# Kernel optimization log

Measured on AMD Instinct MI355X. Metric: run time of the kernel, lower is better.

Reference implementation:

```python
import jax, jax.numpy as jnp
import numpy as np

N = 50000      # total atoms/beads across batch
E = 800000     # total edges (avg degree 16)
H = 128        # hidden_channels
R = 50         # num_rbf
NB = 2         # n_interaction blocks
NG = 64        # num graphs in batch
NT = 100       # num atom types
CUT = 5.0      # upper distance cutoff


def setup_inputs() -> dict:
    key = jax.random.key(0)
    ks = jax.random.split(key, 20)
    atom_types = jax.random.randint(ks[0], (N,), 0, NT)
    pos = jax.random.uniform(ks[1], (N, 3), jnp.float32) * 30.0  # box of 30 Angstrom
    edge_index = jax.random.randint(ks[2], (2, E), 0, N)
    batch = jnp.sort(jax.random.randint(ks[3], (N,), 0, NG))

    def g(k, shape, fan_in):
        return jax.random.normal(k, shape, jnp.float32) * (1.0 / fan_in) ** 0.5

    emb = jax.random.normal(ks[4], (NT, H), jnp.float32) * 0.1
    # filter network per block: Linear(R->H) -> tanh -> Linear(H->H)
    fw1 = g(ks[5], (NB, R, H), R)
    fb1 = jnp.zeros((NB, H), jnp.float32)
    fw2 = g(ks[6], (NB, H, H), H)
    fb2 = jnp.zeros((NB, H), jnp.float32)
    # CFConv lin1 (no bias), lin2 (bias)
    lin1_w = g(ks[7], (NB, H, H), H)
    lin2_w = g(ks[8], (NB, H, H), H)
    lin2_b = jnp.zeros((NB, H), jnp.float32)
    # InteractionBlock output linear
    blk_w = g(ks[9], (NB, H, H), H)
    blk_b = jnp.zeros((NB, H), jnp.float32)
    # output network: Linear(H->H/2) -> tanh -> Linear(H/2->1)
    out_w1 = g(ks[10], (H, H // 2), H)
    out_b1 = jnp.zeros((H // 2,), jnp.float32)
    out_w2 = g(ks[11], (H // 2, 1), H // 2)
    out_b2 = jnp.zeros((1,), jnp.float32)
    return dict(atom_types=atom_types, pos=pos, edge_index=edge_index, batch=batch,
                emb=emb, fw1=fw1, fb1=fb1, fw2=fw2, fb2=fb2,
                lin1_w=lin1_w, lin2_w=lin2_w, lin2_b=lin2_b,
                blk_w=blk_w, blk_b=blk_b,
                out_w1=out_w1, out_b1=out_b1, out_w2=out_w2, out_b2=out_b2)


def reference(atom_types, pos, edge_index, batch, emb, fw1, fb1, fw2, fb2,
              lin1_w, lin2_w, lin2_b, blk_w, blk_b,
              out_w1, out_b1, out_w2, out_b2):
    src, dst = edge_index[0], edge_index[1]
    # pairwise distances along edges (eps keeps sqrt grad finite at coincident points)
    diff = pos[src] - pos[dst]                                  # [E,3]
    d = jnp.sqrt(jnp.sum(diff * diff, axis=-1) + 1e-12)         # [E]
    # Gaussian RBF expansion
    offsets = jnp.linspace(0.0, CUT, R)
    coeff = -0.5 / (offsets[1] - offsets[0]) ** 2
    rbf = jnp.exp(coeff * (d[:, None] - offsets) ** 2)          # [E,R]
    # cosine cutoff envelope
    Cenv = jnp.where(d < CUT, 0.5 * (jnp.cos(d * jnp.pi / CUT) + 1.0), 0.0)  # [E]

    x = emb[atom_types]                                          # [N,H]
    for i in range(NB):
        # filter generation from expanded distances
        W = jnp.tanh(rbf @ fw1[i] + fb1[i]) @ fw2[i] + fb2[i]    # [E,H]
        W = W * Cenv[:, None]
        # CFConv: lin1 -> gather*filter -> scatter-sum -> lin2
        h = x @ lin1_w[i]                                        # [N,H]
        msg = h[src] * W                                         # [E,H]
        agg = jax.ops.segment_sum(msg, dst, num_segments=N)      # [N,H]
        h = agg @ lin2_w[i] + lin2_b[i]
        # InteractionBlock: activation -> lin, residual add in SchNet.forward
        h = jnp.tanh(h)
        x = x + (h @ blk_w[i] + blk_b[i])
    # output network -> per-atom energy, scatter-sum per graph
    e = jnp.tanh(x @ out_w1 + out_b1) @ out_w2 + out_b2          # [N,1]
    energy = jax.ops.segment_sum(e, batch, num_segments=NG)      # [NG,1]
    return energy.flatten()
```

## Files before the change

### kernel.cpp

```cpp
#include <hip/hip_runtime.h>
#include <hip/hip_bf16.h>
#include <math.h>

#define H 128
#define RBF 50
#define CUTF 5.0f
#define PIF 3.14159265358979323846f
#define QT 1024
#define SEG 16

__global__ __launch_bounds__(256) void prep_kernel(
    const float* __restrict__ pos, float4* __restrict__ pos4, int Nn,
    int4* __restrict__ zbase, int zquads,
    const float* __restrict__ fw1, const float* __restrict__ fb1,
    const float* __restrict__ fw2, const float* __restrict__ fb2,
    const float* __restrict__ lin1w, const float* __restrict__ lin2b,
    const float* __restrict__ blkw, const float* __restrict__ blkb,
    const float* __restrict__ emb,
    const float* __restrict__ ow1, const float* __restrict__ ob1,
    const float* __restrict__ ow2, const float* __restrict__ ob2,
    float* __restrict__ tab, float* __restrict__ cvec,
    float* __restrict__ e_type, float* __restrict__ htype0,
    float* __restrict__ htype1, int NT,
    int ZFB, int PB, int FB, int TB, int H0B)
{
    int b = blockIdx.x;
    const int tid = threadIdx.x;
    const int lane = tid & 63;

    if (b < ZFB) {
        int i = b * 256 + tid;
        if (i < zquads) zbase[i] = make_int4(0, 0, 0, 0);
        return;
    }
    b -= ZFB;
    if (b < PB) {
        int n = b * 256 + tid;
        if (n < Nn)
            pos4[n] = make_float4(pos[3 * n], pos[3 * n + 1], pos[3 * n + 2], 0.0f);
        return;
    }
    b -= PB;
    const int h0 = lane, h1 = lane + 64;
    if (b < FB) {
        const int wid = b * 4 + (tid >> 6);
        const int ntab = 2 * (QT + 1);
        if (wid >= ntab + 2) return;
        if (wid >= ntab) {
            const int blk = wid - ntab;
            const float* bwp = blkw + (size_t)blk * H * H;
            float t0 = tanhf(lin2b[blk * H + h0]);
            float t1 = tanhf(lin2b[blk * H + h1]);
            float a0 = blkb[blk * H + h0], a1 = blkb[blk * H + h1];
            #pragma unroll 8
            for (int k = 0; k < 64; ++k) {
                float bb2 = __shfl(t0, k, 64);
                a0 = fmaf(bb2, bwp[k * H + h0], a0);
                a1 = fmaf(bb2, bwp[k * H + h1], a1);
            }
            #pragma unroll 8
            for (int k = 0; k < 64; ++k) {
                float bb2 = __shfl(t1, k, 64);
                a0 = fmaf(bb2, bwp[(64 + k) * H + h0], a0);
                a1 = fmaf(bb2, bwp[(64 + k) * H + h1], a1);
            }
            cvec[blk * H + h0] = a0;
            cvec[blk * H + h1] = a1;
            return;
        }
        const int blk = wid / (QT + 1);
        const int q = wid - blk * (QT + 1);
        const float d = (float)q * (CUTF / (float)QT);
        const float* f1 = fw1 + (size_t)blk * RBF * H;
        const float* f2 = fw2 + (size_t)blk * H * H;
        const float step  = CUTF / 49.0f;
        const float coeff = -0.5f / (step * step);
        float cenv = (d < CUTF) ? 0.5f * (cosf(d * (PIF / CUTF)) + 1.0f) : 0.0f;

        float t0 = fb1[blk * H + h0], t1 = fb1[blk * H + h1];
        #pragma unroll
        for (int r = 0; r < RBF; ++r) {
            float u = d - (float)r * step;
            float rb = expf(coeff * u * u);
            t0 = fmaf(rb, f1[r * H + h0], t0);
            t1 = fmaf(rb, f1[r * H + h1], t1);
        }
        t0 = tanhf(t0); t1 = tanhf(t1);
        float w0 = fb2[blk * H + h0], w1v = fb2[blk * H + h1];
        #pragma unroll 8
        for (int k = 0; k < 64; ++k) {
            float bb2 = __shfl(t0, k, 64);
            w0  = fmaf(bb2, f2[k * H + h0], w0);
            w1v = fmaf(bb2, f2[k * H + h1], w1v);
        }
        #pragma unroll 8
        for (int k = 0; k < 64; ++k) {
            float bb2 = __shfl(t1, k, 64);
            w0  = fmaf(bb2, f2[(64 + k) * H + h0], w0);
            w1v = fmaf(bb2, f2[(64 + k) * H + h1], w1v);
        }
        float* row = tab + ((size_t)blk * (QT + 1) + q) * H;
        row[h0] = w0 * cenv;
        row[h1] = w1v * cenv;
        return;
    }
    b -= FB;
    if (b < TB) {
        const int ty = b * 4 + (tid >> 6);
        if (ty >= NT) return;
        float xt0 = emb[(size_t)ty * H + h0];
        float xt1 = emb[(size_t)ty * H + h1];
        #pragma unroll
        for (int blk = 0; blk < 2; ++blk) {
            const float* bwp = blkw + (size_t)blk * H * H;
            float t0 = tanhf(lin2b[blk * H + h0]);
            float t1 = tanhf(lin2b[blk * H + h1]);
            float a0 = blkb[blk * H + h0], a1 = blkb[blk * H + h1];
            #pragma unroll 8
            for (int k = 0; k < 64; ++k) {
                float bb2 = __shfl(t0, k, 64);
                a0 = fmaf(bb2, bwp[k * H + h0], a0);
                a1 = fmaf(bb2, bwp[k * H + h1], a1);
            }
            #pragma unroll 8
            for (int k = 0; k < 64; ++k) {
                float bb2 = __shfl(t1, k, 64);
                a0 = fmaf(bb2, bwp[(64 + k) * H + h0], a0);
                a1 = fmaf(bb2, bwp[(64 + k) * H + h1], a1);
            }
            xt0 += a0; xt1 += a1;
        }
        float y = ob1[lane];
        #pragma unroll 8
        for (int k = 0; k < 64; ++k) {
            float bb2 = __shfl(xt0, k, 64);
            y = fmaf(bb2, ow1[k * 64 + lane], y);
        }
        #pragma unroll 8
        for (int k = 0; k < 64; ++k) {
            float bb2 = __shfl(xt1, k, 64);
            y = fmaf(bb2, ow1[(64 + k) * 64 + lane], y);
        }
        y = tanhf(y) * ow2[lane];
        #pragma unroll
        for (int off = 32; off; off >>= 1) y += __shfl_xor(y, off, 64);
        if (lane == 0) e_type[ty] = y + ob2[0];
        return;
    }
    b -= TB;
    if (b < H0B) {
        const int ty = b * 4 + (tid >> 6);
        if (ty >= NT) return;
        float x0 = emb[(size_t)ty * H + h0];
        float x1 = emb[(size_t)ty * H + h1];
        float a0 = 0.f, a1 = 0.f;
        #pragma unroll 8
        for (int k = 0; k < 64; ++k) {
            float bb2 = __shfl(x0, k, 64);
            a0 = fmaf(bb2, lin1w[k * H + h0], a0);
            a1 = fmaf(bb2, lin1w[k * H + h1], a1);
        }
        #pragma unroll 8
        for (int k = 0; k < 64; ++k) {
            float bb2 = __shfl(x1, k, 64);
            a0 = fmaf(bb2, lin1w[(64 + k) * H + h0], a0);
            a1 = fmaf(bb2, lin1w[(64 + k) * H + h1], a1);
        }
        htype0[(size_t)ty * H + h0] = a0;
        htype0[(size_t)ty * H + h1] = a1;
        return;
    }
    b -= H0B;
    {
        const int ty = b * 4 + (tid >> 6);
        if (ty >= NT) return;
        const float* bwp = blkw;
        float t0 = tanhf(lin2b[h0]);
        float t1 = tanhf(lin2b[h1]);
        float c0 = blkb[h0], c1 = blkb[h1];
        #pragma unroll 8
        for (int k = 0; k < 64; ++k) {
            float bb2 = __shfl(t0, k, 64);
            c0 = fmaf(bb2, bwp[k * H + h0], c0);
            c1 = fmaf(bb2, bwp[k * H + h1], c1);
        }
        #pragma unroll 8
        for (int k = 0; k < 64; ++k) {
            float bb2 = __shfl(t1, k, 64);
            c0 = fmaf(bb2, bwp[(64 + k) * H + h0], c0);
            c1 = fmaf(bb2, bwp[(64 + k) * H + h1], c1);
        }
        float x0 = emb[(size_t)ty * H + h0] + c0;
        float x1 = emb[(size_t)ty * H + h1] + c1;
        const float* l1 = lin1w + (size_t)H * H;
        float a0 = 0.f, a1 = 0.f;
        #pragma unroll 8
        for (int k = 0; k < 64; ++k) {
            float bb2 = __shfl(x0, k, 64);
            a0 = fmaf(bb2, l1[k * H + h0], a0);
            a1 = fmaf(bb2, l1[k * H + h1], a1);
        }
        #pragma unroll 8
        for (int k = 0; k < 64; ++k) {
            float bb2 = __shfl(x1, k, 64);
            a0 = fmaf(bb2, l1[(64 + k) * H + h0], a0);
            a1 = fmaf(bb2, l1[(64 + k) * H + h1], a1);
        }
        htype1[(size_t)ty * H + h0] = a0;
        htype1[(size_t)ty * H + h1] = a1;
    }
}

__global__ __launch_bounds__(256) void edge_prep_kernel(
    const float4* __restrict__ pos4, const int* __restrict__ ei,
    const int* __restrict__ atype, int E, int CAP,
    int* __restrict__ seg_cnt, int* __restrict__ asrc, int* __restrict__ adst,
    float* __restrict__ ad, int* __restrict__ asty,
    int* __restrict__ is_src, int* __restrict__ is_dst)
{
    __shared__ int wtot[4], wbase[4];
    const int tid = threadIdx.x;
    const int lane = tid & 63;
    const int wv = tid >> 6;
    const int gtid = blockIdx.x * 256 + tid;

    int s[4], t[4];
    float d[4];
    bool act[4] = {false, false, false, false};

    const int e0 = gtid * 4;
    if (e0 + 3 < E && (E & 3) == 0) {
        const int4 sv = *(const int4*)(ei + e0);
        const int4 tv = *(const int4*)(ei + E + e0);
        s[0] = sv.x; s[1] = sv.y; s[2] = sv.z; s[3] = sv.w;
        t[0] = tv.x; t[1] = tv.y; t[2] = tv.z; t[3] = tv.w;
        #pragma unroll
        for (int j = 0; j < 4; ++j) {
            float4 ps = pos4[s[j]], pt = pos4[t[j]];
            float dx = ps.x - pt.x, dy = ps.y - pt.y, dz = ps.z - pt.z;
            d[j] = sqrtf(dx * dx + dy * dy + dz * dz + 1e-12f);
            act[j] = (d[j] < CUTF);
        }
    } else if (e0 < E) {
        #pragma unroll
        for (int j = 0; j < 4; ++j) {
            int e = e0 + j;
            if (e < E) {
                s[j] = ei[e]; t[j] = ei[E + e];
                float4 ps = pos4[s[j]], pt = pos4[t[j]];
                float dx = ps.x - pt.x, dy = ps.y - pt.y, dz = ps.z - pt.z;
                d[j] = sqrtf(dx * dx + dy * dy + dz * dz + 1e-12f);
                act[j] = (d[j] < CUTF);
            }
        }
    }

    unsigned long long b[4];
    int mytot = 0;
    #pragma unroll
    for (int j = 0; j < 4; ++j) {
        b[j] = __ballot(act[j]);
        mytot += (int)__popcll(b[j]);
    }
    if (lane == 0) wtot[wv] = mytot;
    __syncthreads();
    if (tid == 0) {
        int t0 = wtot[0], t1 = wtot[1], t2 = wtot[2], t3 = wtot[3];
        int tot = t0 + t1 + t2 + t3;
        int base = 0;
        if (tot) base = atomicAdd(&seg_cnt[blockIdx.x & (SEG - 1)], tot);
        wbase[0] = base; wbase[1] = base + t0;
        wbase[2] = base + t0 + t1; wbase[3] = base + t0 + t1 + t2;
    }
    __syncthreads();

    int run = wbase[wv];
    const int segoff = (int)(blockIdx.x & (SEG - 1)) * CAP;
    const unsigned long long ltm = ((unsigned long long)1 << lane) - 1;
    #pragma unroll
    for (int j = 0; j < 4; ++j) {
        if (act[j]) {
            int p = segoff + run + (int)__popcll(b[j] & ltm);
            asrc[p] = s[j]; adst[p] = t[j]; ad[p] = d[j];
            asty[p] = atype[s[j]];
            is_src[s[j]] = 1; is_dst[t[j]] = 1;
        }
        run += (int)__popcll(b[j]);
    }
}

__global__ __launch_bounds__(256) void compact_atoms_kernel(
    const int* __restrict__ is_src, const int* __restrict__ is_dst, int Nn,
    int* __restrict__ cnt4,
    int* __restrict__ dst_list, int* __restrict__ sd_list,
    float* __restrict__ agg)
{
    __shared__ int wtot[2][4], wbase[2][4];
    const int tid = threadIdx.x;
    const int lane = tid & 63;
    const int wv = tid >> 6;
    int n = blockIdx.x * 256 + tid;
    bool v[2] = {false, false};
    if (n < Nn) {
        bool vd = is_dst[n] != 0;
        v[0] = vd;
        v[1] = vd && (is_src[n] != 0);
    }
    unsigned long long b[2];
    #pragma unroll
    for (int l = 0; l < 2; ++l) {
        b[l] = __ballot(v[l]);
        if (lane == 0) wtot[l][wv] = (int)__popcll(b[l]);
    }
    __syncthreads();
    if (tid == 0) {
        #pragma unroll
        for (int l = 0; l < 2; ++l) {
            int t0 = wtot[l][0], t1 = wtot[l][1], t2 = wtot[l][2], t3 = wtot[l][3];
            int tot = t0 + t1 + t2 + t3;
            int base = 0;
            if (tot) base = atomicAdd(cnt4 + 1 + l, tot);
            wbase[l][0] = base; wbase[l][1] = base + t0;
            wbase[l][2] = base + t0 + t1; wbase[l][3] = base + t0 + t1 + t2;
        }
    }
    __syncthreads();
    const unsigned long long ltm = ((unsigned long long)1 << lane) - 1;
    if (v[0]) dst_list[wbase[0][wv] + (int)__popcll(b[0] & ltm)] = n;
    if (v[1]) sd_list[wbase[1][wv] + (int)__popcll(b[1] & ltm)] = n;
    if (v[0]) {
        float4 z = make_float4(0.f, 0.f, 0.f, 0.f);
        float4* row = (float4*)(agg + (size_t)n * H);
        #pragma unroll
        for (int c = 0; c < 32; ++c) row[c] = z;
    }
}

__global__ __launch_bounds__(256) void edge_scatter0_kernel(
    const int* __restrict__ seg_cnt,
    const int* __restrict__ adst, const float* __restrict__ ad,
    const int* __restrict__ asty, const float* __restrict__ tab,
    const float* __restrict__ htype0, float* __restrict__ agg, int CAP)
{
    __shared__ int sbase[SEG + 1];
    const int tid = threadIdx.x;
    if (tid == 0) {
        int run = 0;
        #pragma unroll
        for (int s2 = 0; s2 < SEG; ++s2) { sbase[s2] = run; run += seg_cnt[s2]; }
        sbase[SEG] = run;
    }
    __syncthreads();

    const int lane = tid & 63;
    const int wid = (blockIdx.x * blockDim.x + tid) >> 6;
    const int nw  = (gridDim.x * blockDim.x) >> 6;
    const int total = sbase[SEG];
    const float scale = (float)QT / CUTF;

    for (int i = wid; i < total; i += nw) {
        int seg = 0;
        #pragma unroll
        for (int s2 = 1; s2 < SEG; ++s2) seg += (i >= sbase[s2]) ? 1 : 0;
        int slot = seg * CAP + (i - sbase[seg]);

        int t = adst[slot];
        int ty = asty[slot];
        float p = ad[slot] * scale;
        int i0 = (int)p;
        if (i0 > QT - 1) i0 = QT - 1;
        float f = p - (float)i0;
        const float* r0 = tab + (size_t)i0 * H;
        float wl = fmaf(f, r0[H + lane] - r0[lane], r0[lane]);
        float wh = fmaf(f, r0[H + 64 + lane] - r0[64 + lane], r0[64 + lane]);
        const float* hr = htype0 + (size_t)ty * H;
        atomicAdd(agg + (size_t)t * H + lane, hr[lane] * wl);
        atomicAdd(agg + (size_t)t * H + 64 + lane, hr[64 + lane] * wh);
    }
}

__global__ __launch_bounds__(256) void edge_scatter1_kernel(
    const int* __restrict__ seg_cnt,
    const int* __restrict__ asrc, const int* __restrict__ adst,
    const float* __restrict__ ad, const int* __restrict__ asty,
    const int* __restrict__ is_dst, const float* __restrict__ tab,
    const float* __restrict__ hbuf, const float* __restrict__ htype1,
    float* __restrict__ agg, int CAP)
{
    __shared__ int sbase[SEG + 1];
    const int tid = threadIdx.x;
    if (tid == 0) {
        int run = 0;
        #pragma unroll
        for (int s2 = 0; s2 < SEG; ++s2) { sbase[s2] = run; run += seg_cnt[s2]; }
        sbase[SEG] = run;
    }
    __syncthreads();

    const int lane = tid & 63;
    const int wid = (blockIdx.x * blockDim.x + tid) >> 6;
    const int nw  = (gridDim.x * blockDim.x) >> 6;
    const int total = sbase[SEG];
    const float scale = (float)QT / CUTF;

    for (int i = wid; i < total; i += nw) {
        int seg = 0;
        #pragma unroll
        for (int s2 = 1; s2 < SEG; ++s2) seg += (i >= sbase[s2]) ? 1 : 0;
        int slot = seg * CAP + (i - sbase[seg]);

        int s = asrc[slot];
        int t = adst[slot];
        float p = ad[slot] * scale;
        int i0 = (int)p;
        if (i0 > QT - 1) i0 = QT - 1;
        float f = p - (float)i0;
        const float* r0 = tab + (size_t)i0 * H;
        float wl = fmaf(f, r0[H + lane] - r0[lane], r0[lane]);
        float wh = fmaf(f, r0[H + 64 + lane] - r0[64 + lane], r0[64 + lane]);
        const float* hr = is_dst[s] ? (hbuf + (size_t)s * H)
                                    : (htype1 + (size_t)asty[slot] * H);
        atomicAdd(agg + (size_t)t * H + lane, hr[lane] * wl);
        atomicAdd(agg + (size_t)t * H + 64 + lane, hr[64 + lane] * wh);
    }
}

__global__ __launch_bounds__(256) void gemm_sd_kernel(
    const float* __restrict__ A, const float* __restrict__ W,
    float* __restrict__ C,
    const int* __restrict__ rows, const int* __restrict__ cntp)
{
    __shared__ float As[32][36];
    __shared__ float Ws[32][128];
    __shared__ int rlist[32];

    const int tid = threadIdx.x;
    const int cnt = *cntp;
    const int r0 = (tid >> 4) * 2;
    const int c0 = (tid & 15) * 4;

    for (int tile = blockIdx.x; tile * 32 < cnt; tile += gridDim.x) {
        __syncthreads();
        if (tid < 32) {
            int idx = tile * 32 + tid;
            rlist[tid] = (idx < cnt) ? rows[idx] : -1;
        }
        __syncthreads();

        float acc[2][8];
        #pragma unroll
        for (int j = 0; j < 2; ++j)
            #pragma unroll
            for (int c = 0; c < 8; ++c) acc[j][c] = 0.f;

        for (int kc = 0; kc < H; kc += 32) {
            {
                int lr = tid >> 3;
                int kk = (tid & 7) * 4;
                int r = rlist[lr];
                float4 v = make_float4(0.f, 0.f, 0.f, 0.f);
                if (r >= 0) v = *(const float4*)(A + (size_t)r * H + kc + kk);
                *(float4*)&As[lr][kk] = v;
            }
            {
                int wr = tid >> 5;
                int wc = (tid & 31) * 4;
                #pragma unroll
                for (int p = 0; p < 4; ++p) {
                    int row = wr + p * 8;
                    *(float4*)&Ws[row][wc] = *(const float4*)(W + (size_t)(kc + row) * H + wc);
                }
            }
            __syncthreads();
            #pragma unroll
            for (int k = 0; k < 32; k += 4) {
                float a_[2][4];
                #pragma unroll
                for (int j = 0; j < 2; ++j)
                    *(float4*)a_[j] = *(const float4*)&As[r0 + j][k];
                #pragma unroll
                for (int kk = 0; kk < 4; ++kk) {
                    float4 wlo = *(const float4*)&Ws[k + kk][c0];
                    float4 whi = *(const float4*)&Ws[k + kk][c0 + 64];
                    float w_[8] = {wlo.x, wlo.y, wlo.z, wlo.w, whi.x, whi.y, whi.z, whi.w};
                    #pragma unroll
                    for (int j = 0; j < 2; ++j)
                        #pragma unroll
                        for (int c = 0; c < 8; ++c)
                            acc[j][c] = fmaf(a_[j][kk], w_[c], acc[j][c]);
                }
            }
            __syncthreads();
        }
        #pragma unroll
        for (int j = 0; j < 2; ++j) {
            int r = rlist[r0 + j];
            if (r < 0) continue;
            #pragma unroll
            for (int hh = 0; hh < 2; ++hh) {
                int cb = c0 + hh * 64;
                *(float4*)(C + (size_t)r * H + cb) = make_float4(
                    acc[j][hh * 4 + 0], acc[j][hh * 4 + 1],
                    acc[j][hh * 4 + 2], acc[j][hh * 4 + 3]);
            }
        }
    }
}

__global__ __launch_bounds__(256) void update_x0_kernel(
    float* __restrict__ agg, const float* __restrict__ l2w,
    const float* __restrict__ l2b, const float* __restrict__ bw,
    const float* __restrict__ bb, float* __restrict__ x,
    const float* __restrict__ emb, const int* __restrict__ atype,
    const int* __restrict__ rows, const int* __restrict__ cntp)
{
    __shared__ float As[32][36];
    __shared__ float Ws[32][128];
    __shared__ float Tl[32][132];
    __shared__ int rlist[32], tlist[32];

    const int tid = threadIdx.x;
    const int cnt = *cntp;
    const int r0 = (tid >> 4) * 2;
    const int c0 = (tid & 15) * 4;

    for (int tile = blockIdx.x; tile * 32 < cnt; tile += gridDim.x) {
        __syncthreads();
        if (tid < 32) {
            int idx = tile * 32 + tid;
            int r = (idx < cnt) ? rows[idx] : -1;
            rlist[tid] = r;
            tlist[tid] = (r >= 0) ? atype[r] : 0;
        }
        __syncthreads();

        float acc[2][8];
        #pragma unroll
        for (int j = 0; j < 2; ++j)
            #pragma unroll
            for (int c = 0; c < 8; ++c) acc[j][c] = 0.f;

        for (int kc = 0; kc < H; kc += 32) {
            {
                int lr = tid >> 3;
                int kk = (tid & 7) * 4;
                int r = rlist[lr];
                float4 v = make_float4(0.f, 0.f, 0.f, 0.f);
                if (r >= 0) v = *(const float4*)(agg + (size_t)r * H + kc + kk);
                *(float4*)&As[lr][kk] = v;
            }
            {
                int wr = tid >> 5;
                int wc = (tid & 31) * 4;
                #pragma unroll
                for (int p = 0; p < 4; ++p) {
                    int row = wr + p * 8;
                    *(float4*)&Ws[row][wc] = *(const float4*)(l2w + (size_t)(kc + row) * H + wc);
                }
            }
            __syncthreads();
            #pragma unroll
            for (int k = 0; k < 32; k += 4) {
                float a_[2][4];
                #pragma unroll
                for (int j = 0; j < 2; ++j)
                    *(float4*)a_[j] = *(const float4*)&As[r0 + j][k];
                #pragma unroll
                for (int kk = 0; kk < 4; ++kk) {
                    float4 wlo = *(const float4*)&Ws[k + kk][c0];
                    float4 whi = *(const float4*)&Ws[k + kk][c0 + 64];
                    float w_[8] = {wlo.x, wlo.y, wlo.z, wlo.w, whi.x, whi.y, whi.z, whi.w};
                    #pragma unroll
                    for (int j = 0; j < 2; ++j)
                        #pragma unroll
                        for (int c = 0; c < 8; ++c)
                            acc[j][c] = fmaf(a_[j][kk], w_[c], acc[j][c]);
                }
            }
            __syncthreads();
        }
        {
            float4 z = make_float4(0.f, 0.f, 0.f, 0.f);
            for (int idx = tid; idx < 32 * 32; idx += 256) {
                int row = idx >> 5, c = (idx & 31) << 2;
                int r = rlist[row];
                if (r >= 0) *(float4*)(agg + (size_t)r * H + c) = z;
            }
        }
        #pragma unroll
        for (int j = 0; j < 2; ++j) {
            float4 lo, hi;
            lo.x = tanhf(acc[j][0] + l2b[c0]);      lo.y = tanhf(acc[j][1] + l2b[c0 + 1]);
            lo.z = tanhf(acc[j][2] + l2b[c0 + 2]);  lo.w = tanhf(acc[j][3] + l2b[c0 + 3]);
            hi.x = tanhf(acc[j][4] + l2b[c0 + 64]); hi.y = tanhf(acc[j][5] + l2b[c0 + 65]);
            hi.z = tanhf(acc[j][6] + l2b[c0 + 66]); hi.w = tanhf(acc[j][7] + l2b[c0 + 67]);
            *(float4*)&Tl[r0 + j][c0] = lo;
            *(float4*)&Tl[r0 + j][c0 + 64] = hi;
        }

        float acc2[2][8];
        #pragma unroll
        for (int j = 0; j < 2; ++j)
            #pragma unroll
            for (int c = 0; c < 8; ++c) acc2[j][c] = 0.f;

        for (int kc = 0; kc < H; kc += 32) {
            __syncthreads();
            {
                int wr = tid >> 5;
                int wc = (tid & 31) * 4;
                #pragma unroll
                for (int p = 0; p < 4; ++p) {
                    int row = wr + p * 8;
                    *(float4*)&Ws[row][wc] = *(const float4*)(bw + (size_t)(kc + row) * H + wc);
                }
            }
            __syncthreads();
            #pragma unroll
            for (int k = 0; k < 32; k += 4) {
                float a_[2][4];
                #pragma unroll
                for (int j = 0; j < 2; ++j)
                    *(float4*)a_[j] = *(const float4*)&Tl[r0 + j][kc + k];
                #pragma unroll
                for (int kk = 0; kk < 4; ++kk) {
                    float4 wlo = *(const float4*)&Ws[k + kk][c0];
                    float4 whi = *(const float4*)&Ws[k + kk][c0 + 64];
                    float w_[8] = {wlo.x, wlo.y, wlo.z, wlo.w, whi.x, whi.y, whi.z, whi.w};
                    #pragma unroll
                    for (int j = 0; j < 2; ++j)
                        #pragma unroll
                        for (int c = 0; c < 8; ++c)
                            acc2[j][c] = fmaf(a_[j][kk], w_[c], acc2[j][c]);
                }
            }
        }
        #pragma unroll
        for (int j = 0; j < 2; ++j) {
            int r = rlist[r0 + j];
            if (r < 0) continue;
            int ty = tlist[r0 + j];
            #pragma unroll
            for (int hh = 0; hh < 2; ++hh) {
                int cb = c0 + hh * 64;
                float4 xv = *(const float4*)(emb + (size_t)ty * H + cb);
                xv.x += acc2[j][hh * 4 + 0] + bb[cb];
                xv.y += acc2[j][hh * 4 + 1] + bb[cb + 1];
                xv.z += acc2[j][hh * 4 + 2] + bb[cb + 2];
                xv.w += acc2[j][hh * 4 + 3] + bb[cb + 3];
                *(float4*)(x + (size_t)r * H + cb) = xv;
            }
        }
    }
}

__global__ __launch_bounds__(256) void update_e_kernel(
    const float* __restrict__ agg, const float* __restrict__ l2w,
    const float* __restrict__ l2b, const float* __restrict__ bw,
    const float* __restrict__ bb, const float* __restrict__ x,
    const float* __restrict__ ow1, const float* __restrict__ ob1,
    const float* __restrict__ ow2, const float* __restrict__ ob2,
    float* __restrict__ e_atom,
    const int* __restrict__ rows, const int* __restrict__ cntp)
{
    __shared__ float As[32][36];
    __shared__ float Ws[32][128];
    __shared__ float Tl[32][132];
    __shared__ int rlist[32];

    const int tid = threadIdx.x;
    const int cnt = *cntp;
    const int r0 = (tid >> 4) * 2;
    const int c0 = (tid & 15) * 4;

    for (int tile = blockIdx.x; tile * 32 < cnt; tile += gridDim.x) {
        __syncthreads();
        if (tid < 32) {
            int idx = tile * 32 + tid;
            rlist[tid] = (idx < cnt) ? rows[idx] : -1;
        }
        __syncthreads();

        float acc[2][8];
        #pragma unroll
        for (int j = 0; j < 2; ++j)
            #pragma unroll
            for (int c = 0; c < 8; ++c) acc[j][c] = 0.f;

        for (int kc = 0; kc < H; kc += 32) {
            {
                int lr = tid >> 3;
                int kk = (tid & 7) * 4;
                int r = rlist[lr];
                float4 v = make_float4(0.f, 0.f, 0.f, 0.f);
                if (r >= 0) v = *(const float4*)(agg + (size_t)r * H + kc + kk);
                *(float4*)&As[lr][kk] = v;
            }
            {
                int wr = tid >> 5;
                int wc = (tid & 31) * 4;
                #pragma unroll
                for (int p = 0; p < 4; ++p) {
                    int row = wr + p * 8;
                    *(float4*)&Ws[row][wc] = *(const float4*)(l2w + (size_t)(kc + row) * H + wc);
                }
            }
            __syncthreads();
            #pragma unroll
            for (int k = 0; k < 32; k += 4) {
                float a_[2][4];
                #pragma unroll
                for (int j = 0; j < 2; ++j)
                    *(float4*)a_[j] = *(const float4*)&As[r0 + j][k];
                #pragma unroll
                for (int kk = 0; kk < 4; ++kk) {
                    float4 wlo = *(const float4*)&Ws[k + kk][c0];
                    float4 whi = *(const float4*)&Ws[k + kk][c0 + 64];
                    float w_[8] = {wlo.x, wlo.y, wlo.z, wlo.w, whi.x, whi.y, whi.z, whi.w};
                    #pragma unroll
                    for (int j = 0; j < 2; ++j)
                        #pragma unroll
                        for (int c = 0; c < 8; ++c)
                            acc[j][c] = fmaf(a_[j][kk], w_[c], acc[j][c]);
                }
            }
            __syncthreads();
        }
        #pragma unroll
        for (int j = 0; j < 2; ++j) {
            float4 lo, hi;
            lo.x = tanhf(acc[j][0] + l2b[c0]);      lo.y = tanhf(acc[j][1] + l2b[c0 + 1]);
            lo.z = tanhf(acc[j][2] + l2b[c0 + 2]);  lo.w = tanhf(acc[j][3] + l2b[c0 + 3]);
            hi.x = tanhf(acc[j][4] + l2b[c0 + 64]); hi.y = tanhf(acc[j][5] + l2b[c0 + 65]);
            hi.z = tanhf(acc[j][6] + l2b[c0 + 66]); hi.w = tanhf(acc[j][7] + l2b[c0 + 67]);
            *(float4*)&Tl[r0 + j][c0] = lo;
            *(float4*)&Tl[r0 + j][c0 + 64] = hi;
        }

        float acc2[2][8];
        #pragma unroll
        for (int j = 0; j < 2; ++j)
            #pragma unroll
            for (int c = 0; c < 8; ++c) acc2[j][c] = 0.f;

        for (int kc = 0; kc < H; kc += 32) {
            __syncthreads();
            {
                int wr = tid >> 5;
                int wc = (tid & 31) * 4;
                #pragma unroll
                for (int p = 0; p < 4; ++p) {
                    int row = wr + p * 8;
                    *(float4*)&Ws[row][wc] = *(const float4*)(bw + (size_t)(kc + row) * H + wc);
                }
            }
            __syncthreads();
            #pragma unroll
            for (int k = 0; k < 32; k += 4) {
                float a_[2][4];
                #pragma unroll
                for (int j = 0; j < 2; ++j)
                    *(float4*)a_[j] = *(const float4*)&Tl[r0 + j][kc + k];
                #pragma unroll
                for (int kk = 0; kk < 4; ++kk) {
                    float4 wlo = *(const float4*)&Ws[k + kk][c0];
                    float4 whi = *(const float4*)&Ws[k + kk][c0 + 64];
                    float w_[8] = {wlo.x, wlo.y, wlo.z, wlo.w, whi.x, whi.y, whi.z, whi.w};
                    #pragma unroll
                    for (int j = 0; j < 2; ++j)
                        #pragma unroll
                        for (int c = 0; c < 8; ++c)
                            acc2[j][c] = fmaf(a_[j][kk], w_[c], acc2[j][c]);
                }
            }
        }
        __syncthreads();
        #pragma unroll
        for (int j = 0; j < 2; ++j) {
            int r = rlist[r0 + j];
            #pragma unroll
            for (int hh = 0; hh < 2; ++hh) {
                int cb = c0 + hh * 64;
                float4 xv = make_float4(0.f, 0.f, 0.f, 0.f);
                if (r >= 0) xv = *(const float4*)(x + (size_t)r * H + cb);
                xv.x += acc2[j][hh * 4 + 0] + bb[cb];
                xv.y += acc2[j][hh * 4 + 1] + bb[cb + 1];
                xv.z += acc2[j][hh * 4 + 2] + bb[cb + 2];
                xv.w += acc2[j][hh * 4 + 3] + bb[cb + 3];
                *(float4*)&Tl[r0 + j][cb] = xv;
            }
        }

        float acc3[2][4];
        #pragma unroll
        for (int j = 0; j < 2; ++j)
            #pragma unroll
            for (int c = 0; c < 4; ++c) acc3[j][c] = 0.f;

        for (int kc = 0; kc < H; kc += 32) {
            __syncthreads();
            {
                int wr = tid >> 4;
                int wc = (tid & 15) * 4;
                #pragma unroll
                for (int p = 0; p < 2; ++p) {
                    int row = wr + p * 16;
                    *(float4*)&Ws[row][wc] = *(const float4*)(ow1 + (size_t)(kc + row) * 64 + wc);
                }
            }
            __syncthreads();
            #pragma unroll
            for (int k = 0; k < 32; ++k) {
                float a_[2];
                #pragma unroll
                for (int j = 0; j < 2; ++j) a_[j] = Tl[r0 + j][kc + k];
                float4 wv = *(const float4*)&Ws[k][c0];
                #pragma unroll
                for (int j = 0; j < 2; ++j) {
                    acc3[j][0] = fmaf(a_[j], wv.x, acc3[j][0]);
                    acc3[j][1] = fmaf(a_[j], wv.y, acc3[j][1]);
                    acc3[j][2] = fmaf(a_[j], wv.z, acc3[j][2]);
                    acc3[j][3] = fmaf(a_[j], wv.w, acc3[j][3]);
                }
            }
        }
        const float4 b1v = *(const float4*)(ob1 + c0);
        const float4 w2v = *(const float4*)(ow2 + c0);
        float ep[2];
        #pragma unroll
        for (int j = 0; j < 2; ++j) {
            float v0 = tanhf(acc3[j][0] + b1v.x);
            float v1 = tanhf(acc3[j][1] + b1v.y);
            float v2 = tanhf(acc3[j][2] + b1v.z);
            float v3 = tanhf(acc3[j][3] + b1v.w);
            ep[j] = v0 * w2v.x + v1 * w2v.y + v2 * w2v.z + v3 * w2v.w;
        }
        #pragma unroll
        for (int off = 1; off < 16; off <<= 1) {
            ep[0] += __shfl_xor(ep[0], off, 64);
            ep[1] += __shfl_xor(ep[1], off, 64);
        }
        if ((tid & 15) == 0) {
            const float b2v = ob2[0];
            #pragma unroll
            for (int j = 0; j < 2; ++j) {
                int r = rlist[r0 + j];
                if (r >= 0) e_atom[r] = ep[j] + b2v;
            }
        }
    }
}

__global__ __launch_bounds__(256) void energy_graph_kernel(
    const int* __restrict__ batch, const int* __restrict__ atype,
    const int* __restrict__ is_dst, const float* __restrict__ e_atom,
    const float* __restrict__ e_type, float* __restrict__ energy, int Nn)
{
    const int g = blockIdx.x;
    int lo = 0, hi = Nn;
    while (lo < hi) { int m = (lo + hi) >> 1; if (batch[m] < g) lo = m + 1; else hi = m; }
    const int start = lo;
    hi = Nn;
    while (lo < hi) { int m = (lo + hi) >> 1; if (batch[m] < g + 1) lo = m + 1; else hi = m; }
    const int end = lo;

    float s = 0.0f;
    for (int n = start + (int)threadIdx.x; n < end; n += 256)
        s += is_dst[n] ? e_atom[n] : e_type[atype[n]];
    #pragma unroll
    for (int off = 32; off; off >>= 1) s += __shfl_xor(s, off, 64);
    __shared__ float wp[4];
    if ((threadIdx.x & 63) == 0) wp[threadIdx.x >> 6] = s;
    __syncthreads();
    if (threadIdx.x == 0) energy[g] = wp[0] + wp[1] + wp[2] + wp[3];
}

extern "C" void kernel_launch(void* const* d_in, const int* in_sizes, int n_in,
                              void* d_out, int out_size, void* d_ws, size_t ws_size,
                              hipStream_t stream)
{
    const int*   atype = (const int*)  d_in[0];
    const float* pos   = (const float*)d_in[1];
    const int*   ei    = (const int*)  d_in[2];
    const int*   batch = (const int*)  d_in[3];
    const float* emb   = (const float*)d_in[4];
    const float* fw1   = (const float*)d_in[5];
    const float* fb1   = (const float*)d_in[6];
    const float* fw2   = (const float*)d_in[7];
    const float* fb2   = (const float*)d_in[8];
    const float* lin1w = (const float*)d_in[9];
    const float* lin2w = (const float*)d_in[10];
    const float* lin2b = (const float*)d_in[11];
    const float* blkw  = (const float*)d_in[12];
    const float* blkb  = (const float*)d_in[13];
    const float* ow1   = (const float*)d_in[14];
    const float* ob1   = (const float*)d_in[15];
    const float* ow2   = (const float*)d_in[16];
    const float* ob2   = (const float*)d_in[17];

    const int Nn = in_sizes[0];
    const int E  = in_sizes[2] / 2;
    const int NT = in_sizes[4] / H;
    float* energy = (float*)d_out;

    const int eblocks = (E + 1023) / 1024;
    const int bps = (eblocks + SEG - 1) / SEG;
    const int CAP = bps * 1024;
    const int SEGCAP = SEG * CAP;

    char* w = (char*)d_ws;
    int*   cnt  = (int*)w;
    int*   seg_cnt = cnt + 8;
    int*   is_src = cnt + 32;
    int*   is_dst = is_src + Nn;
    float* x    = (float*)(is_dst + Nn);
    float* hbuf = x + (size_t)Nn * H;
    float* agg  = hbuf + (size_t)Nn * H;
    int*   asrc = (int*)(agg + (size_t)Nn * H);
    int*   adst = asrc + SEGCAP;
    float* ad   = (float*)(adst + SEGCAP);
    int*   asty = (int*)(ad + SEGCAP);
    int*   dst_list = asty + SEGCAP;
    int*   sd_list  = dst_list + Nn;
    float* cvec = (float*)(sd_list + Nn);
    float* tab  = cvec + 2 * H;
    float* e_type = tab + 2 * (size_t)(QT + 1) * H;
    float* htype0 = e_type + 128;
    float* htype1 = htype0 + (size_t)NT * H;
    float* e_atom = htype1 + (size_t)NT * H;
    float4* pos4 = (float4*)(e_atom + Nn);

    const int zquads = (128 + 2 * Nn * 4) / 16;
    const int ZFB = (zquads + 255) / 256;
    const int PB  = (Nn + 255) / 256;
    const int FB  = (2 * (QT + 1) + 2 + 3) / 4;
    const int TB  = (NT + 3) / 4;
    const int H0B = (NT + 3) / 4;
    const int H1B = (NT + 3) / 4;

    prep_kernel<<<ZFB + PB + FB + TB + H0B + H1B, 256, 0, stream>>>(
        pos, pos4, Nn, (int4*)cnt, zquads,
        fw1, fb1, fw2, fb2, lin1w, lin2b, blkw, blkb, emb,
        ow1, ob1, ow2, ob2, tab, cvec, e_type, htype0, htype1, NT,
        ZFB, PB, FB, TB, H0B);

    edge_prep_kernel<<<eblocks, 256, 0, stream>>>(
        pos4, ei, atype, E, CAP, seg_cnt, asrc, adst, ad, asty, is_src, is_dst);
    compact_atoms_kernel<<<(Nn + 255) / 256, 256, 0, stream>>>(
        is_src, is_dst, Nn, cnt, dst_list, sd_list, agg);

    edge_scatter0_kernel<<<1024, 256, 0, stream>>>(
        seg_cnt, adst, ad, asty, tab, htype0, agg, CAP);
    update_x0_kernel<<<512, 256, 0, stream>>>(
        agg, lin2w, lin2b, blkw, blkb, x, emb, atype, dst_list, cnt + 1);

    gemm_sd_kernel<<<128, 256, 0, stream>>>(
        x, lin1w + (size_t)H * H, hbuf, sd_list, cnt + 2);
    edge_scatter1_kernel<<<1024, 256, 0, stream>>>(
        seg_cnt, asrc, adst, ad, asty, is_dst,
        tab + (size_t)(QT + 1) * H, hbuf, htype1, agg, CAP);
    update_e_kernel<<<512, 256, 0, stream>>>(
        agg, lin2w + (size_t)H * H, lin2b + H, blkw + (size_t)H * H, blkb + H,
        x, ow1, ob1, ow2, ob2, e_atom, dst_list, cnt + 1);

    energy_graph_kernel<<<out_size, 256, 0, stream>>>(
        batch, atype, is_dst, e_atom, e_type, energy, Nn);
}
```

Before: 223.2 us.

## Fuse atom compaction into scatter0 and lin1 GEMM into update_x0

Merges compact_atoms into the first edge-scatter launch as extra blocks, and moves zeroing of agg into the prep kernel's bulk zero-fill. Fuses the block-1 lin1 GEMM (x @ lin1_w) into update_x0, so the freshly updated x tile is reused from shared memory instead of being re-read by a separate gemm_sd kernel. Removes the unused cvec precompute. This cuts two kernel launches and one N×H read of x, at the cost of zero-filling all of agg (not just dst rows) and extra work for atoms that are not sources.

```diff
diff --git a/kernel.cpp b/kernel.cpp
--- a/kernel.cpp
+++ b/kernel.cpp
@@ -8,6 +8,7 @@
 #define PIF 3.14159265358979323846f
 #define QT 1024
 #define SEG 16
+#define SB 1024
 
 __global__ __launch_bounds__(256) void prep_kernel(
     const float* __restrict__ pos, float4* __restrict__ pos4, int Nn,
@@ -19,9 +20,8 @@
     const float* __restrict__ emb,
     const float* __restrict__ ow1, const float* __restrict__ ob1,
     const float* __restrict__ ow2, const float* __restrict__ ob2,
-    float* __restrict__ tab, float* __restrict__ cvec,
-    float* __restrict__ e_type, float* __restrict__ htype0,
-    float* __restrict__ htype1, int NT,
+    float* __restrict__ tab, float* __restrict__ e_type,
+    float* __restrict__ htype0, float* __restrict__ htype1, int NT,
     int ZFB, int PB, int FB, int TB, int H0B)
 {
     int b = blockIdx.x;
@@ -45,29 +45,7 @@
     if (b < FB) {
         const int wid = b * 4 + (tid >> 6);
         const int ntab = 2 * (QT + 1);
-        if (wid >= ntab + 2) return;
-        if (wid >= ntab) {
-            const int blk = wid - ntab;
-            const float* bwp = blkw + (size_t)blk * H * H;
-            float t0 = tanhf(lin2b[blk * H + h0]);
-            float t1 = tanhf(lin2b[blk * H + h1]);
-            float a0 = blkb[blk * H + h0], a1 = blkb[blk * H + h1];
-            #pragma unroll 8
-            for (int k = 0; k < 64; ++k) {
-                float bb2 = __shfl(t0, k, 64);
-                a0 = fmaf(bb2, bwp[k * H + h0], a0);
-                a1 = fmaf(bb2, bwp[k * H + h1], a1);
-            }
-            #pragma unroll 8
-            for (int k = 0; k < 64; ++k) {
-                float bb2 = __shfl(t1, k, 64);
-                a0 = fmaf(bb2, bwp[(64 + k) * H + h0], a0);
-                a1 = fmaf(bb2, bwp[(64 + k) * H + h1], a1);
-            }
-            cvec[blk * H + h0] = a0;
-            cvec[blk * H + h1] = a1;
-            return;
-        }
+        if (wid >= ntab) return;
         const int blk = wid / (QT + 1);
         const int q = wid - blk * (QT + 1);
         const float d = (float)q * (CUTF / (float)QT);
@@ -289,61 +267,53 @@
     }
 }
 
-__global__ __launch_bounds__(256) void compact_atoms_kernel(
-    const int* __restrict__ is_src, const int* __restrict__ is_dst, int Nn,
-    int* __restrict__ cnt4,
-    int* __restrict__ dst_list, int* __restrict__ sd_list,
-    float* __restrict__ agg)
-{
-    __shared__ int wtot[2][4], wbase[2][4];
-    const int tid = threadIdx.x;
-    const int lane = tid & 63;
-    const int wv = tid >> 6;
-    int n = blockIdx.x * 256 + tid;
-    bool v[2] = {false, false};
-    if (n < Nn) {
-        bool vd = is_dst[n] != 0;
-        v[0] = vd;
-        v[1] = vd && (is_src[n] != 0);
-    }
-    unsigned long long b[2];
-    #pragma unroll
-    for (int l = 0; l < 2; ++l) {
-        b[l] = __ballot(v[l]);
-        if (lane == 0) wtot[l][wv] = (int)__popcll(b[l]);
-    }
-    __syncthreads();
-    if (tid == 0) {
-        #pragma unroll
-        for (int l = 0; l < 2; ++l) {
-            int t0 = wtot[l][0], t1 = wtot[l][1], t2 = wtot[l][2], t3 = wtot[l][3];
-            int tot = t0 + t1 + t2 + t3;
-            int base = 0;
-            if (tot) base = atomicAdd(cnt4 + 1 + l, tot);
-            wbase[l][0] = base; wbase[l][1] = base + t0;
-            wbase[l][2] = base + t0 + t1; wbase[l][3] = base + t0 + t1 + t2;
-        }
-    }
-    __syncthreads();
-    const unsigned long long ltm = ((unsigned long long)1 << lane) - 1;
-    if (v[0]) dst_list[wbase[0][wv] + (int)__popcll(b[0] & ltm)] = n;
-    if (v[1]) sd_list[wbase[1][wv] + (int)__popcll(b[1] & ltm)] = n;
-    if (v[0]) {
-        float4 z = make_float4(0.f, 0.f, 0.f, 0.f);
-        float4* row = (float4*)(agg + (size_t)n * H);
-        #pragma unroll
-        for (int c = 0; c < 32; ++c) row[c] = z;
-    }
-}
-
-__global__ __launch_bounds__(256) void edge_scatter0_kernel(
+__global__ __launch_bounds__(256) void scatter0_compact_kernel(
     const int* __restrict__ seg_cnt,
     const int* __restrict__ adst, const float* __restrict__ ad,
     const int* __restrict__ asty, const float* __restrict__ tab,
-    const float* __restrict__ htype0, float* __restrict__ agg, int CAP)
+    const float* __restrict__ htype0, float* __restrict__ agg, int CAP,
+    const int* __restrict__ is_src, const int* __restrict__ is_dst, int Nn,
+    int* __restrict__ cnt4, int* __restrict__ dst_list, int* __restrict__ sd_list)
 {
+    const int tid = threadIdx.x;
+    const int lane = tid & 63;
+
+    if (blockIdx.x >= SB) {
+        __shared__ int wtot[2][4], wbase[2][4];
+        const int wv = tid >> 6;
+        int n = ((int)blockIdx.x - SB) * 256 + tid;
+        bool v[2] = {false, false};
+        if (n < Nn) {
+            bool vd = is_dst[n] != 0;
+            v[0] = vd;
+            v[1] = vd && (is_src[n] != 0);
+        }
+        unsigned long long b[2];
+        #pragma unroll
+        for (int l = 0; l < 2; ++l) {
+            b[l] = __ballot(v[l]);
+            if (lane == 0) wtot[l][wv] = (int)__popcll(b[l]);
+        }
+        __syncthreads();
+        if (tid == 0) {
+            #pragma unroll
+            for (int l = 0; l < 2; ++l) {
+                int t0 = wtot[l][0], t1 = wtot[l][1], t2 = wtot[l][2], t3 = wtot[l][3];
+                int tot = t0 + t1 + t2 + t3;
+                int base = 0;
+                if (tot) base = atomicAdd(cnt4 + 1 + l, tot);
+                wbase[l][0] = base; wbase[l][1] = base + t0;
+                wbase[l][2] = base + t0 + t1; wbase[l][3] = base + t0 + t1 + t2;
+            }
+        }
+        __syncthreads();
+        const unsigned long long ltm = ((unsigned long long)1 << lane) - 1;
+        if (v[0]) dst_list[wbase[0][wv] + (int)__popcll(b[0] & ltm)] = n;
+        if (v[1]) sd_list[wbase[1][wv] + (int)__popcll(b[1] & ltm)] = n;
+        return;
+    }
+
     __shared__ int sbase[SEG + 1];
-    const int tid = threadIdx.x;
     if (tid == 0) {
         int run = 0;
         #pragma unroll
@@ -352,9 +322,8 @@
     }
     __syncthreads();
 
-    const int lane = tid & 63;
     const int wid = (blockIdx.x * blockDim.x + tid) >> 6;
-    const int nw  = (gridDim.x * blockDim.x) >> 6;
+    const int nw  = (SB * 256) >> 6;
     const int total = sbase[SEG];
     const float scale = (float)QT / CUTF;
 
@@ -425,14 +394,19 @@
     }
 }
 
-__global__ __launch_bounds__(256) void gemm_sd_kernel(
-    const float* __restrict__ A, const float* __restrict__ W,
-    float* __restrict__ C,
+__global__ __launch_bounds__(256) void update_x0_kernel(
+    float* __restrict__ agg, const float* __restrict__ l2w,
+    const float* __restrict__ l2b, const float* __restrict__ bw,
+    const float* __restrict__ bb, float* __restrict__ x,
+    const float* __restrict__ emb, const int* __restrict__ atype,
+    const int* __restrict__ is_src, const float* __restrict__ l1w1,
+    float* __restrict__ hbuf,
     const int* __restrict__ rows, const int* __restrict__ cntp)
 {
     __shared__ float As[32][36];
     __shared__ float Ws[32][128];
-    __shared__ int rlist[32];
+    __shared__ float Tl[32][132];
+    __shared__ int rlist[32], tlist[32], slist[32];
 
     const int tid = threadIdx.x;
     const int cnt = *cntp;
@@ -443,7 +417,10 @@
         __syncthreads();
         if (tid < 32) {
             int idx = tile * 32 + tid;
-            rlist[tid] = (idx < cnt) ? rows[idx] : -1;
+            int r = (idx < cnt) ? rows[idx] : -1;
+            rlist[tid] = r;
+            tlist[tid] = (r >= 0) ? atype[r] : 0;
+            slist[tid] = (r >= 0) ? is_src[r] : 0;
         }
         __syncthreads();
 
@@ -459,7 +436,7 @@
                 int kk = (tid & 7) * 4;
                 int r = rlist[lr];
                 float4 v = make_float4(0.f, 0.f, 0.f, 0.f);
-                if (r >= 0) v = *(const float4*)(A + (size_t)r * H + kc + kk);
+                if (r >= 0) v = *(const float4*)(agg + (size_t)r * H + kc + kk);
                 *(float4*)&As[lr][kk] = v;
             }
             {
@@ -468,7 +445,7 @@
                 #pragma unroll
                 for (int p = 0; p < 4; ++p) {
                     int row = wr + p * 8;
-                    *(float4*)&Ws[row][wc] = *(const float4*)(W + (size_t)(kc + row) * H + wc);
+                    *(float4*)&Ws[row][wc] = *(const float4*)(l2w + (size_t)(kc + row) * H + wc);
                 }
             }
             __syncthreads();
@@ -492,93 +469,6 @@
             }
             __syncthreads();
         }
-        #pragma unroll
-        for (int j = 0; j < 2; ++j) {
-            int r = rlist[r0 + j];
-            if (r < 0) continue;
-            #pragma unroll
-            for (int hh = 0; hh < 2; ++hh) {
-                int cb = c0 + hh * 64;
-                *(float4*)(C + (size_t)r * H + cb) = make_float4(
-                    acc[j][hh * 4 + 0], acc[j][hh * 4 + 1],
-                    acc[j][hh * 4 + 2], acc[j][hh * 4 + 3]);
-            }
-        }
-    }
-}
-
-__global__ __launch_bounds__(256) void update_x0_kernel(
-    float* __restrict__ agg, const float* __restrict__ l2w,
-    const float* __restrict__ l2b, const float* __restrict__ bw,
-    const float* __restrict__ bb, float* __restrict__ x,
-    const float* __restrict__ emb, const int* __restrict__ atype,
-    const int* __restrict__ rows, const int* __restrict__ cntp)
-{
-    __shared__ float As[32][36];
-    __shared__ float Ws[32][128];
-    __shared__ float Tl[32][132];
-    __shared__ int rlist[32], tlist[32];
-
-    const int tid = threadIdx.x;
-    const int cnt = *cntp;
-    const int r0 = (tid >> 4) * 2;
-    const int c0 = (tid & 15) * 4;
-
-    for (int tile = blockIdx.x; tile * 32 < cnt; tile += gridDim.x) {
-        __syncthreads();
-        if (tid < 32) {
-            int idx = tile * 32 + tid;
-            int r = (idx < cnt) ? rows[idx] : -1;
-            rlist[tid] = r;
-            tlist[tid] = (r >= 0) ? atype[r] : 0;
-        }
-        __syncthreads();
-
-        float acc[2][8];
-        #pragma unroll
-        for (int j = 0; j < 2; ++j)
-            #pragma unroll
-            for (int c = 0; c < 8; ++c) acc[j][c] = 0.f;
-
-        for (int kc = 0; kc < H; kc += 32) {
-            {
-                int lr = tid >> 3;
-                int kk = (tid & 7) * 4;
-                int r = rlist[lr];
-                float4 v = make_float4(0.f, 0.f, 0.f, 0.f);
-                if (r >= 0) v = *(const float4*)(agg + (size_t)r * H + kc + kk);
-                *(float4*)&As[lr][kk] = v;
-            }
-            {
-                int wr = tid >> 5;
-                int wc = (tid & 31) * 4;
-                #pragma unroll
-                for (int p = 0; p < 4; ++p) {
-                    int row = wr + p * 8;
-                    *(float4*)&Ws[row][wc] = *(const float4*)(l2w + (size_t)(kc + row) * H + wc);
-                }
-            }
-            __syncthreads();
-            #pragma unroll
-            for (int k = 0; k < 32; k += 4) {
-                float a_[2][4];
-                #pragma unroll
-                for (int j = 0; j < 2; ++j)
-                    *(float4*)a_[j] = *(const float4*)&As[r0 + j][k];
-                #pragma unroll
-                for (int kk = 0; kk < 4; ++kk) {
-                    float4 wlo = *(const float4*)&Ws[k + kk][c0];
-                    float4 whi = *(const float4*)&Ws[k + kk][c0 + 64];
-                    float w_[8] = {wlo.x, wlo.y, wlo.z, wlo.w, whi.x, whi.y, whi.z, whi.w};
-                    #pragma unroll
-                    for (int j = 0; j < 2; ++j)
-                        #pragma unroll
-                        for (int c = 0; c < 8; ++c)
-                            acc[j][c] = fmaf(a_[j][kk], w_[c], acc[j][c]);
-                }
-            }
-            __syncthreads();
-        }
         {
             float4 z = make_float4(0.f, 0.f, 0.f, 0.f);
             for (int idx = tid; idx < 32 * 32; idx += 256) {
@@ -635,20 +525,72 @@
                 }
             }
         }
+        __syncthreads();
         #pragma unroll
         for (int j = 0; j < 2; ++j) {
             int r = rlist[r0 + j];
-            if (r < 0) continue;
             int ty = tlist[r0 + j];
             #pragma unroll
             for (int hh = 0; hh < 2; ++hh) {
                 int cb = c0 + hh * 64;
-                float4 xv = *(const float4*)(emb + (size_t)ty * H + cb);
+                float4 xv = make_float4(0.f, 0.f, 0.f, 0.f);
+                if (r >= 0) xv = *(const float4*)(emb + (size_t)ty * H + cb);
                 xv.x += acc2[j][hh * 4 + 0] + bb[cb];
                 xv.y += acc2[j][hh * 4 + 1] + bb[cb + 1];
                 xv.z += acc2[j][hh * 4 + 2] + bb[cb + 2];
                 xv.w += acc2[j][hh * 4 + 3] + bb[cb + 3];
-                *(float4*)(x + (size_t)r * H + cb) = xv;
+                *(float4*)&Tl[r0 + j][cb] = xv;
+                if (r >= 0) *(float4*)(x + (size_t)r * H + cb) = xv;
+            }
+        }
+
+        float acc3[2][8];
+        #pragma unroll
+        for (int j = 0; j < 2; ++j)
+            #pragma unroll
+            for (int c = 0; c < 8; ++c) acc3[j][c] = 0.f;
+
+        for (int kc = 0; kc < H; kc += 32) {
+            __syncthreads();
+            {
+                int wr = tid >> 5;
+                int wc = (tid & 31) * 4;
+                #pragma unroll
+                for (int p = 0; p < 4; ++p) {
+                    int row = wr + p * 8;
+                    *(float4*)&Ws[row][wc] = *(const float4*)(l1w1 + (size_t)(kc + row) * H + wc);
+                }
+            }
+            __syncthreads();
+            #pragma unroll
+            for (int k = 0; k < 32; k += 4) {
+                float a_[2][4];
+                #pragma unroll
+                for (int j = 0; j < 2; ++j)
+                    *(float4*)a_[j] = *(const float4*)&Tl[r0 + j][kc + k];
+                #pragma unroll
+                for (int kk = 0; kk < 4; ++kk) {
+                    float4 wlo = *(const float4*)&Ws[k + kk][c0];
+                    float4 whi = *(const float4*)&Ws[k + kk][c0 + 64];
+                    float w_[8] = {wlo.x, wlo.y, wlo.z, wlo.w, whi.x, whi.y, whi.z, whi.w};
+                    #pragma unroll
+                    for (int j = 0; j < 2; ++j)
+                        #pragma unroll
+                        for (int c = 0; c < 8; ++c)
+                            acc3[j][c] = fmaf(a_[j][kk], w_[c], acc3[j][c]);
+                }
+            }
+        }
+        #pragma unroll
+        for (int j = 0; j < 2; ++j) {
+            int r = rlist[r0 + j];
+            if (r < 0 || !slist[r0 + j]) continue;
+            #pragma unroll
+            for (int hh = 0; hh < 2; ++hh) {
+                int cb = c0 + hh * 64;
+                *(float4*)(hbuf + (size_t)r * H + cb) = make_float4(
+                    acc3[j][hh * 4 + 0], acc3[j][hh * 4 + 1],
+                    acc3[j][hh * 4 + 2], acc3[j][hh * 4 + 3]);
             }
         }
     }
@@ -913,27 +855,27 @@
     int*   seg_cnt = cnt + 8;
     int*   is_src = cnt + 32;
     int*   is_dst = is_src + Nn;
-    float* x    = (float*)(is_dst + Nn);
+    float* agg  = (float*)(is_dst + Nn);
+    float* x    = agg + (size_t)Nn * H;
     float* hbuf = x + (size_t)Nn * H;
-    float* agg  = hbuf + (size_t)Nn * H;
-    int*   asrc = (int*)(agg + (size_t)Nn * H);
+    int*   asrc = (int*)(hbuf + (size_t)Nn * H);
     int*   adst = asrc + SEGCAP;
     float* ad   = (float*)(adst + SEGCAP);
     int*   asty = (int*)(ad + SEGCAP);
     int*   dst_list = asty + SEGCAP;
     int*   sd_list  = dst_list + Nn;
-    float* cvec = (float*)(sd_list + Nn);
-    float* tab  = cvec + 2 * H;
+    float* tab  = (float*)(sd_list + Nn);
     float* e_type = tab + 2 * (size_t)(QT + 1) * H;
     float* htype0 = e_type + 128;
     float* htype1 = htype0 + (size_t)NT * H;
     float* e_atom = htype1 + (size_t)NT * H;
     float4* pos4 = (float4*)(e_atom + Nn);
 
-    const int zquads = (128 + 2 * Nn * 4) / 16;
+    const size_t zbytes = 128 + 2 * (size_t)Nn * 4 + (size_t)Nn * H * 4;
+    const int zquads = (int)(zbytes / 16);
     const int ZFB = (zquads + 255) / 256;
     const int PB  = (Nn + 255) / 256;
-    const int FB  = (2 * (QT + 1) + 2 + 3) / 4;
+    const int FB  = (2 * (QT + 1) + 3) / 4;
     const int TB  = (NT + 3) / 4;
     const int H0B = (NT + 3) / 4;
     const int H1B = (NT + 3) / 4;
@@ -941,21 +883,22 @@
     prep_kernel<<<ZFB + PB + FB + TB + H0B + H1B, 256, 0, stream>>>(
         pos, pos4, Nn, (int4*)cnt, zquads,
         fw1, fb1, fw2, fb2, lin1w, lin2b, blkw, blkb, emb,
-        ow1, ob1, ow2, ob2, tab, cvec, e_type, htype0, htype1, NT,
+        ow1, ob1, ow2, ob2, tab, e_type, htype0, htype1, NT,
         ZFB, PB, FB, TB, H0B);
 
     edge_prep_kernel<<<eblocks, 256, 0, stream>>>(
         pos4, ei, atype, E, CAP, seg_cnt, asrc, adst, ad, asty, is_src, is_dst);
-    compact_atoms_kernel<<<(Nn + 255) / 256, 256, 0, stream>>>(
-        is_src, is_dst, Nn, cnt, dst_list, sd_list, agg);
-
-    edge_scatter0_kernel<<<1024, 256, 0, stream>>>(
-        seg_cnt, adst, ad, asty, tab, htype0, agg, CAP);
+
+    {
+        int CB = (Nn + 255) / 256;
+        scatter0_compact_kernel<<<SB + CB, 256, 0, stream>>>(
+            seg_cnt, adst, ad, asty, tab, htype0, agg, CAP,
+            is_src, is_dst, Nn, cnt, dst_list, sd_list);
+    }
     update_x0_kernel<<<512, 256, 0, stream>>>(
-        agg, lin2w, lin2b, blkw, blkb, x, emb, atype, dst_list, cnt + 1);
-
-    gemm_sd_kernel<<<128, 256, 0, stream>>>(
-        x, lin1w + (size_t)H * H, hbuf, sd_list, cnt + 2);
+        agg, lin2w, lin2b, blkw, blkb, x, emb, atype,
+        is_src, lin1w + (size_t)H * H, hbuf, dst_list, cnt + 1);
+
     edge_scatter1_kernel<<<1024, 256, 0, stream>>>(
         seg_cnt, asrc, adst, ad, asty, is_dst,
         tab + (size_t)(QT + 1) * H, hbuf, htype1, agg, CAP);
```

New measurement: 224.8 us. No clear change (+0.7%).
